# Optimization experiments

Hardware: AMD Instinct MI355X
Metric: run time of the kernel (lower is better)

## Reference

```python
import jax, jax.numpy as jnp
import numpy as np

B, N = 16, 512
CFL = 0.5


def _conv(x, k):
    return jax.lax.conv_general_dilated(x, k, (1, 1), 'VALID', dimension_numbers=('NHWC', 'HWIO', 'NHWC'))


def _pad(x, p):  # p = (top, bottom, left, right) spatial pads
    return jnp.pad(x, ((0, 0), (p[0], p[1]), (p[2], p[3]), (0, 0)))


def _t(k):  # transpose(perm=[1,0,2,3]) on an HWIO kernel
    return jnp.transpose(k, (1, 0, 2, 3))


def _amper(E, Hx, Hy, beta, delta, fb, fd, fy, kf, kb, fu, fdn):
    n = N
    s1 = (_pad(beta * _conv(Hy, _t(fb)) + delta * _conv(Hy, _t(fd)) + _conv(Hy, _t(fy)), (2, 2, 2, 2))
          + _pad(_conv(Hy, _t(kf)), (2, 2, 0, n - 1))
          + _pad(_conv(Hy, _t(kb)), (2, 2, n - 1, 0))
          + _pad(_conv(Hy, _t(fu)), (2, 2, 1, n - 2))
          + _pad(_conv(Hy, _t(fdn)), (2, 2, n - 2, 1)))
    s2 = (_pad(beta * _conv(Hx, fb) + delta * _conv(Hx, fd) + _conv(Hx, fy), (2, 2, 2, 2))
          + _pad(_conv(Hx, kf), (0, n - 1, 2, 2))
          + _pad(_conv(Hx, kb), (n - 1, 0, 2, 2))
          + _pad(_conv(Hx, fu), (1, n - 2, 2, 2))
          + _pad(_conv(Hx, fdn), (n - 2, 1, 2, 2)))
    return E + CFL * (s1 - s2)


def _faraday(E, Hx, Hy, beta, delta, fb, fd, fy, kef, keb):
    n = N
    s3 = (_pad(beta * _conv(E, fb) + delta * _conv(E, fd) + _conv(E, fy), (0, 0, 1, 1))
          + _pad(_conv(E, kef), (1, 1, 0, n - 2))[:, 1:-1, :, :]
          + _pad(_conv(E, keb), (1, 1, n - 2, 0))[:, 1:-1, :, :])
    s4 = (_pad(beta * _conv(E, _t(fb)) + delta * _conv(E, _t(fd)) + _conv(E, _t(fy)), (1, 1, 0, 0))
          + _pad(_conv(E, _t(kef)), (0, n - 2, 1, 1))[:, :, 1:-1, :]
          + _pad(_conv(E, _t(keb)), (n - 2, 0, 1, 1))[:, :, 1:-1, :])
    return Hx - CFL * s3, Hy + CFL * s4


def _forward(E1, Hx1, Hy1, beta, delta, fb, fd, fy, kf, kb, fu, fdn, kef, keb):
    E2 = _amper(E1, Hx1, Hy1, beta, delta, fb, fd, fy, kf, kb, fu, fdn)
    Hx2, Hy2 = _faraday(E2, Hx1, Hy1, beta, delta, fb, fd, fy, kef, keb)
    E3 = _amper(E2, Hx2, Hy2, beta, delta, fb, fd, fy, kf, kb, fu, fdn)
    Hx3, Hy3 = _faraday(E3, Hx2, Hy2, beta, delta, fb, fd, fy, kef, keb)
    E4 = _amper(E3, Hx3, Hy3, beta, delta, fb, fd, fy, kf, kb, fu, fdn)
    Hx4, Hy4 = _faraday(E4, Hx3, Hy3, beta, delta, fb, fd, fy, kef, keb)
    return (E2, Hx2, Hy2, E3, Hx3, Hy3, E4, Hx4, Hy4)


def setup_inputs():
    key = jax.random.key(0)
    ks = jax.random.split(key, 16)
    f32 = jnp.float32
    E_shape, Hx_shape, Hy_shape = (B, N + 1, N + 1, 1), (B, N - 1, N, 1), (B, N, N - 1, 1)
    # interior 2D DRP stencils (3x4): 4-tap staggered derivative x 3-tap transverse weights
    fy = np.zeros((3, 4, 1, 1), np.float32)
    fy[1, 1, 0, 0] = -1.0
    fy[1, 2, 0, 0] = 1.0
    fb = (np.outer([1.0, -2.0, 1.0], [0.0, -1.0, 1.0, 0.0]) / 8.0).astype(np.float32).reshape(3, 4, 1, 1)
    fd = (np.outer([0.0, 1.0, 0.0], [1.0, -3.0, 3.0, -1.0]) / 24.0).astype(np.float32).reshape(3, 4, 1, 1)
    rnd = lambda k, s: 0.05 * jax.random.normal(k, s, dtype=f32)
    return {
        'E1': jax.random.normal(ks[0], E_shape, f32),
        'Hx1': jax.random.normal(ks[1], Hx_shape, f32),
        'Hy1': jax.random.normal(ks[2], Hy_shape, f32),
        'E2': jax.random.normal(ks[3], E_shape, f32),
        'Hx2': jax.random.normal(ks[4], Hx_shape, f32),
        'Hy2': jax.random.normal(ks[5], Hy_shape, f32),
        'E3': jax.random.normal(ks[6], E_shape, f32),
        'Hx3': jax.random.normal(ks[7], Hx_shape, f32),
        'Hy3': jax.random.normal(ks[8], Hy_shape, f32),
        'beta': jnp.zeros((), f32),
        'delta': jnp.asarray([0.37], f32),
        'filter_beta': jnp.asarray(fb),
        'filter_delta': jnp.asarray(fd),
        'filter_yee': jnp.asarray(fy),
        'kernel_forward': rnd(ks[9], (N - 2, 4, 1, 1)),
        'kernel_backward': rnd(ks[10], (N - 2, 4, 1, 1)),
        'fourth_up': rnd(ks[11], (N - 2, 4, 1, 1)),
        'fourth_down': rnd(ks[12], (N - 2, 4, 1, 1)),
        'kernel_e_forward': rnd(ks[13], (3, N, 1, 1)),
        'kernel_e_backward': rnd(ks[14], (3, N, 1, 1)),
    }


def reference(E1, Hx1, Hy1, E2, Hx2, Hy2, E3, Hx3, Hy3, beta, delta, filter_beta, filter_delta, filter_yee, kernel_forward, kernel_backward, fourth_up, fourth_down, kernel_e_forward, kernel_e_backward):
    # Note: the original layer unpacks E2..Hy3 but never uses them.
    return _forward(E1, Hx1, Hy1, beta, delta, filter_beta, filter_delta, filter_yee,
                    kernel_forward, kernel_backward, fourth_up, fourth_down,
                    kernel_e_forward, kernel_e_backward)
```

## Files before the change

### kernel.cpp

```cpp
#include <hip/hip_runtime.h>

#define NB 16
#define NN 512
#define NP 513
#define NM 511
#define CFLc 0.5f

#define SE (NP*NP)
#define SHX (NM*NN)
#define SHY (NN*NM)

#define WS_BIG 0
#define WS_SMALL (16*16*6*512)
#define WS_TOT (WS_SMALL + 16*512*6)

__device__ __forceinline__ float dot4(float4 a, float4 b) {
    return a.x*b.x + a.y*b.y + a.z*b.z + a.w*b.w;
}

__device__ __forceinline__ void ld5(const float* __restrict__ a, int mb, float4* cr) {
    const float4* a4 = (const float4*)a;
    #pragma unroll
    for (int t = 0; t < 5; t++) {
        int idx = mb - 1 + t;
        if (idx >= 0 && idx <= 509) cr[t] = a4[idx];
        else cr[t] = make_float4(0.f, 0.f, 0.f, 0.f);
    }
}

__global__ __launch_bounds__(512, 4) void k_step1(
    const float* __restrict__ E, const float* __restrict__ Hx, const float* __restrict__ Hy,
    const float* __restrict__ beta, const float* __restrict__ delta,
    const float* __restrict__ fb, const float* __restrict__ fd, const float* __restrict__ fy,
    const float* __restrict__ kf, const float* __restrict__ kb,
    const float* __restrict__ fu, const float* __restrict__ fdn,
    float* __restrict__ ws, float* __restrict__ Eout)
{
    __shared__ float s_hy[7][512];
    __shared__ float s_hx[6][512];
    __shared__ float s_strip[8][6];
    __shared__ float gsm[12];

    int bid = blockIdx.x;
    int tid = threadIdx.x;

    if (bid < 256) {
        int b = bid >> 4;
        int chunk = bid & 15;
        int j = tid;
        if (j > 508) return;
        int p0 = chunk * 32;
        int p1 = min(510, p0 + 32);
        const float* Hxb = Hx + (size_t)b*SHX;
        float akf0=0,akf1=0,akb0=0,akb1=0,afu0=0,afu1=0,afd0=0,afd1=0;
        float r0v[4], r1v[4];
        #pragma unroll
        for (int q = 0; q < 4; q++) r0v[q] = Hxb[(size_t)p0*NN + j + q];
        for (int p = p0; p < p1; p++) {
            #pragma unroll
            for (int q = 0; q < 4; q++) r1v[q] = Hxb[(size_t)(p+1)*NN + j + q];
            #pragma unroll
            for (int q = 0; q < 4; q++) {
                float ckf = kf[p*4+q], ckb = kb[p*4+q], cfu = fu[p*4+q], cfd = fdn[p*4+q];
                akf0 += r0v[q]*ckf; akf1 += r1v[q]*ckf;
                akb0 += r0v[q]*ckb; akb1 += r1v[q]*ckb;
                afu0 += r0v[q]*cfu; afu1 += r1v[q]*cfu;
                afd0 += r0v[q]*cfd; afd1 += r1v[q]*cfd;
            }
            #pragma unroll
            for (int q = 0; q < 4; q++) r0v[q] = r1v[q];
        }
        float* o = ws + WS_BIG + (((size_t)b*16 + chunk)*6)*512 + j;
        o[0*512] = akf0;
        o[1*512] = akf1 + afu0;
        o[2*512] = afu1;
        o[3*512] = afd0;
        o[4*512] = afd1 + akb0;
        o[5*512] = akb1;
        return;
    }

    int wrk = bid - 256;
    wrk = (wrk & 7) * 258 + (wrk >> 3);
    int rg = wrk >> 4;
    int b  = wrk & 15;
    int r0 = rg * 4;

    const float* Eb  = E  + (size_t)b*SE;
    const float* Hxb = Hx + (size_t)b*SHX;
    const float* Hyb = Hy + (size_t)b*SHY;
    int c = tid;

    if (tid < 12) gsm[tid] = beta[0]*fb[tid] + delta[0]*fd[tid] + fy[tid];
    #pragma unroll
    for (int k = 0; k < 7; k++) {
        int rm = min(max(r0-2+k, 0), 511);
        s_hy[k][c] = Hyb[(size_t)rm*NM + min(c, 510)];
    }
    #pragma unroll
    for (int k = 0; k < 6; k++) {
        int rm = min(max(r0-2+k, 0), 510);
        s_hx[k][c] = Hxb[(size_t)rm*NN + c];
    }
    __syncthreads();

    {
        int w = tid >> 6, lane = tid & 63;
        int jj = w >> 1;
        int ii = r0 + jj - 2;
        if (ii >= 0 && ii <= 508) {
            int h = w & 1;
            int mb = h*256 + lane*4;
            float4 hv0 = *(const float4*)&s_hy[jj+0][mb];
            float4 hv1 = *(const float4*)&s_hy[jj+1][mb];
            float4 hv2 = *(const float4*)&s_hy[jj+2][mb];
            float4 hv3 = *(const float4*)&s_hy[jj+3][mb];
            float4 hc0 = make_float4(hv0.x, hv1.x, hv2.x, hv3.x);
            float4 hc1 = make_float4(hv0.y, hv1.y, hv2.y, hv3.y);
            float4 hc2 = make_float4(hv0.z, hv1.z, hv2.z, hv3.z);
            float4 hc3 = make_float4(hv0.w, hv1.w, hv2.w, hv3.w);
            float4 cr[5];
            ld5(kf, mb, cr);
            float pkf0 = dot4(hc0,cr[1]) + dot4(hc1,cr[2]) + dot4(hc2,cr[3]) + dot4(hc3,cr[4]);
            float pkf1 = dot4(hc0,cr[0]) + dot4(hc1,cr[1]) + dot4(hc2,cr[2]) + dot4(hc3,cr[3]);
            ld5(fu, mb, cr);
            float pfu0 = dot4(hc0,cr[1]) + dot4(hc1,cr[2]) + dot4(hc2,cr[3]) + dot4(hc3,cr[4]);
            float pfu1 = dot4(hc0,cr[0]) + dot4(hc1,cr[1]) + dot4(hc2,cr[2]) + dot4(hc3,cr[3]);
            ld5(fdn, mb, cr);
            float pfd0 = dot4(hc0,cr[1]) + dot4(hc1,cr[2]) + dot4(hc2,cr[3]) + dot4(hc3,cr[4]);
            float pfd1 = dot4(hc0,cr[0]) + dot4(hc1,cr[1]) + dot4(hc2,cr[2]) + dot4(hc3,cr[3]);
            ld5(kb, mb, cr);
            float pkb0 = dot4(hc0,cr[1]) + dot4(hc1,cr[2]) + dot4(hc2,cr[3]) + dot4(hc3,cr[4]);
            float pkb1 = dot4(hc0,cr[0]) + dot4(hc1,cr[1]) + dot4(hc2,cr[2]) + dot4(hc3,cr[3]);
            float v0 = pkf0;
            float v1 = pkf1 + pfu0;
            float v2 = pfu1;
            float v3 = pfd0;
            float v4 = pfd1 + pkb0;
            float v5 = pkb1;
            #pragma unroll
            for (int off = 32; off > 0; off >>= 1) {
                v0 += __shfl_down(v0, off);
                v1 += __shfl_down(v1, off);
                v2 += __shfl_down(v2, off);
                v3 += __shfl_down(v3, off);
                v4 += __shfl_down(v4, off);
                v5 += __shfl_down(v5, off);
            }
            if (lane == 0) {
                s_strip[w][0]=v0; s_strip[w][1]=v1; s_strip[w][2]=v2;
                s_strip[w][3]=v3; s_strip[w][4]=v4; s_strip[w][5]=v5;
            }
        }
    }
    __syncthreads();

    float g[12];
    #pragma unroll
    for (int i = 0; i < 12; i++) g[i] = gsm[i];

    int cy0 = min(max(c-2,0),510), cy1 = min(max(c-1,0),510), cy2 = min(c,510);
    int cx0 = max(c-2,0), cx1 = max(c-1,0), cx3 = min(c+1,511);
    float hyv[7][3];
    #pragma unroll
    for (int k = 0; k < 7; k++) {
        hyv[k][0]=s_hy[k][cy0]; hyv[k][1]=s_hy[k][cy1]; hyv[k][2]=s_hy[k][cy2];
    }
    float hxv[6][4];
    #pragma unroll
    for (int k = 0; k < 6; k++) {
        hxv[k][0]=s_hx[k][cx0]; hxv[k][1]=s_hx[k][cx1]; hxv[k][2]=s_hx[k][c]; hxv[k][3]=s_hx[k][cx3];
    }

    bool cint = (c >= 2 && c <= 510);
    int cslot = (c==0)?0:(c==1)?1:(c==2)?2:(c==510)?3:(c==511)?4:-1;
    float* Eo = Eout + (size_t)b*SE;

    #pragma unroll
    for (int j2 = 0; j2 < 4; j2++) {
        int r = r0 + j2;
        if (r > 512) break;
        float v = Eb[(size_t)r*NP + c];
        bool rint = (r >= 2 && r <= 510);
        if (rint && cint) {
            float s1 = 0.f, s2 = 0.f;
            #pragma unroll
            for (int p = 0; p < 4; p++)
                s1 += g[p]*hyv[j2+p][0] + g[4+p]*hyv[j2+p][1] + g[8+p]*hyv[j2+p][2];
            #pragma unroll
            for (int p = 0; p < 3; p++)
                s2 += g[p*4+0]*hxv[j2+p][0] + g[p*4+1]*hxv[j2+p][1]
                    + g[p*4+2]*hxv[j2+p][2] + g[p*4+3]*hxv[j2+p][3];
            v += CFLc * (s1 - s2);
        }
        if (rint && cslot >= 0)
            v += CFLc * (s_strip[2*j2][cslot] + s_strip[2*j2+1][cslot]);
        Eo[(size_t)r*NP + c] = v;
        if (c == 511) {
            float v2 = Eb[(size_t)r*NP + 512];
            if (rint) v2 += CFLc * (s_strip[2*j2][5] + s_strip[2*j2+1][5]);
            Eo[(size_t)r*NP + 512] = v2;
        }
    }
}

__global__ __launch_bounds__(512) void k_fix_e(
    const float* __restrict__ ws, float* __restrict__ Eout)
{
    int b = blockIdx.y;
    int which = blockIdx.x;
    int r = (which < 3) ? which : 507 + which;
    int c = 2 + threadIdx.x;
    if (c > 510) return;
    float s = 0.f;
    #pragma unroll
    for (int ch = 0; ch < 16; ch++)
        s += ws[WS_BIG + (((size_t)b*16 + ch)*6 + which)*512 + (c-2)];
    Eout[(size_t)b*SE + (size_t)r*NP + c] -= CFLc * s;
}

__global__ __launch_bounds__(512, 4) void k_step2(
    const float* __restrict__ E, const float* __restrict__ Hx, const float* __restrict__ Hy,
    const float* __restrict__ beta, const float* __restrict__ delta,
    const float* __restrict__ fb, const float* __restrict__ fd, const float* __restrict__ fy,
    const float* __restrict__ kef, const float* __restrict__ keb,
    float* __restrict__ ws, float* __restrict__ Hxout, float* __restrict__ Hyout)
{
    __shared__ float s_e[7][520];
    __shared__ float s_strip2[8][4];
    __shared__ float gsm[12];

    int bid = blockIdx.x;
    int tid = threadIdx.x;

    if (bid < 256) {
        int b = bid >> 4, chunk = bid & 15;
        int c = tid;
        if (c > 510) return;
        int p0 = chunk*32, p1 = p0 + 32;
        const float* Eb = E + (size_t)b*SE;
        float af0=0, af1=0, ab0=0, ab1=0;
        float r0v[3], r1v[3];
        #pragma unroll
        for (int q = 0; q < 3; q++) r0v[q] = Eb[(size_t)p0*NP + c + q];
        for (int p = p0; p < p1; p++) {
            #pragma unroll
            for (int q = 0; q < 3; q++) r1v[q] = Eb[(size_t)(p+1)*NP + c + q];
            float cf0 = kef[p], cf1 = kef[512+p], cf2 = kef[1024+p];
            float cb0 = keb[p], cb1 = keb[512+p], cb2 = keb[1024+p];
            af0 += r0v[0]*cf0 + r0v[1]*cf1 + r0v[2]*cf2;
            af1 += r1v[0]*cf0 + r1v[1]*cf1 + r1v[2]*cf2;
            ab0 += r0v[0]*cb0 + r0v[1]*cb1 + r0v[2]*cb2;
            ab1 += r1v[0]*cb0 + r1v[1]*cb1 + r1v[2]*cb2;
            r0v[0]=r1v[0]; r0v[1]=r1v[1]; r0v[2]=r1v[2];
        }
        float* o = ws + WS_BIG + (((size_t)b*16 + chunk)*4)*512 + c;
        o[0*512] = af0; o[1*512] = af1; o[2*512] = ab0; o[3*512] = ab1;
        return;
    }

    if (tid < 12) gsm[tid] = beta[0]*fb[tid] + delta[0]*fd[tid] + fy[tid];
    int c = tid;

    if (bid < 2304) {
        int wrk = bid - 256;
        wrk = (wrk & 7)*256 + (wrk >> 3);
        int y = wrk >> 4, b = wrk & 15;
        int r0 = y*4;
        const float* Eb = E + (size_t)b*SE;
        #pragma unroll
        for (int k = 0; k < 6; k++) {
            int rm = min(r0+k, 512);
            s_e[k][c] = Eb[(size_t)rm*NP + c];
            if (c == 511) s_e[k][512] = Eb[(size_t)rm*NP + 512];
        }
        __syncthreads();

        {
            int w = tid >> 6, lane = tid & 63;
            int jj = w >> 1, h = w & 1;
            int rr = r0 + jj;
            if (rr <= 510) {
                int mb = h*256 + lane*4;
                int q4 = mb >> 2;
                float4 e0 = *(const float4*)&s_e[jj+0][mb];
                float4 e1 = *(const float4*)&s_e[jj+1][mb];
                float4 e2 = *(const float4*)&s_e[jj+2][mb];
                const float4* kef4 = (const float4*)kef;
                const float4* keb4 = (const float4*)keb;
                float4 f0 = kef4[q4], f1 = kef4[128+q4], f2 = kef4[256+q4];
                float4 b0 = keb4[q4], b1 = keb4[128+q4], b2 = keb4[256+q4];
                float af0 = dot4(e0,f0) + dot4(e1,f1) + dot4(e2,f2);
                float ab0 = dot4(e0,b0) + dot4(e1,b1) + dot4(e2,b2);
                float pw0 = (mb >= 1) ? kef[mb-1]      : 0.f;
                float pw1 = (mb >= 1) ? kef[512+mb-1]  : 0.f;
                float pw2 = (mb >= 1) ? kef[1024+mb-1] : 0.f;
                float af1 = dot4(e0, make_float4(pw0, f0.x, f0.y, f0.z))
                          + dot4(e1, make_float4(pw1, f1.x, f1.y, f1.z))
                          + dot4(e2, make_float4(pw2, f2.x, f2.y, f2.z));
                pw0 = (mb >= 1) ? keb[mb-1]      : 0.f;
                pw1 = (mb >= 1) ? keb[512+mb-1]  : 0.f;
                pw2 = (mb >= 1) ? keb[1024+mb-1] : 0.f;
                float ab1 = dot4(e0, make_float4(pw0, b0.x, b0.y, b0.z))
                          + dot4(e1, make_float4(pw1, b1.x, b1.y, b1.z))
                          + dot4(e2, make_float4(pw2, b2.x, b2.y, b2.z));
                if (mb == 508) {
                    float e512_0 = s_e[jj+0][512];
                    float e512_1 = s_e[jj+1][512];
                    float e512_2 = s_e[jj+2][512];
                    af1 += e512_0*kef[511] + e512_1*kef[1023] + e512_2*kef[1535];
                    ab1 += e512_0*keb[511] + e512_1*keb[1023] + e512_2*keb[1535];
                }
                #pragma unroll
                for (int off = 32; off > 0; off >>= 1) {
                    af0 += __shfl_down(af0, off);
                    af1 += __shfl_down(af1, off);
                    ab0 += __shfl_down(ab0, off);
                    ab1 += __shfl_down(ab1, off);
                }
                if (lane == 0) {
                    s_strip2[w][0]=af0; s_strip2[w][1]=af1;
                    s_strip2[w][2]=ab0; s_strip2[w][3]=ab1;
                }
            }
        }
        __syncthreads();

        float g[12];
        #pragma unroll
        for (int i = 0; i < 12; i++) g[i] = gsm[i];
        int c0 = max(c-1,0), c2i = min(c+1,512), c3i = min(c+2,512);
        float ev[6][4];
        #pragma unroll
        for (int k = 0; k < 6; k++) {
            ev[k][0]=s_e[k][c0]; ev[k][1]=s_e[k][c]; ev[k][2]=s_e[k][c2i]; ev[k][3]=s_e[k][c3i];
        }
        bool cint = (c >= 1 && c <= 510);
        int slot = (c==0)?0:(c==1)?1:(c==510)?2:(c==511)?3:-1;
        const float* Hxb = Hx + (size_t)b*SHX;
        float* Ho = Hxout + (size_t)b*SHX;
        #pragma unroll
        for (int j2 = 0; j2 < 4; j2++) {
            int r = r0 + j2;
            if (r > 510) break;
            float v = Hxb[(size_t)r*NN + c];
            if (cint) {
                float s = 0.f;
                #pragma unroll
                for (int p = 0; p < 3; p++)
                    s += g[p*4+0]*ev[j2+p][0] + g[p*4+1]*ev[j2+p][1]
                       + g[p*4+2]*ev[j2+p][2] + g[p*4+3]*ev[j2+p][3];
                v -= CFLc * s;
            }
            if (slot >= 0)
                v -= CFLc * (s_strip2[2*j2][slot] + s_strip2[2*j2+1][slot]);
            Ho[(size_t)r*NN + c] = v;
        }
    } else {
        int wrk = bid - 2304;
        wrk = (wrk & 7)*256 + (wrk >> 3);
        int y = wrk >> 4, b = wrk & 15;
        int r0 = y*4;
        const float* Eb = E + (size_t)b*SE;
        #pragma unroll
        for (int k = 0; k < 7; k++) {
            int rm = min(max(r0-1+k, 0), 512);
            s_e[k][c] = Eb[(size_t)rm*NP + c];
            if (c == 511) s_e[k][512] = Eb[(size_t)rm*NP + 512];
        }
        __syncthreads();
        if (c > 510) return;

        float g[12];
        #pragma unroll
        for (int i = 0; i < 12; i++) g[i] = gsm[i];
        float ev[7][3];
        #pragma unroll
        for (int k = 0; k < 7; k++) {
            ev[k][0]=s_e[k][c]; ev[k][1]=s_e[k][c+1]; ev[k][2]=s_e[k][c+2];
        }
        const float* Hyb = Hy + (size_t)b*SHY;
        float* Ho = Hyout + (size_t)b*SHY;
        #pragma unroll
        for (int j2 = 0; j2 < 4; j2++) {
            int r = r0 + j2;
            float v = Hyb[(size_t)r*NM + c];
            if (r >= 1 && r <= 510) {
                float s = 0.f;
                #pragma unroll
                for (int p = 0; p < 4; p++)
                    s += g[p]*ev[j2+p][0] + g[4+p]*ev[j2+p][1] + g[8+p]*ev[j2+p][2];
                v += CFLc * s;
            }
            Ho[(size_t)r*NM + c] = v;
        }
    }
}

__global__ __launch_bounds__(512) void k_fix_hy(
    const float* __restrict__ ws, float* __restrict__ Hyout)
{
    int b = blockIdx.y;
    int which = blockIdx.x;
    int r = (which < 2) ? which : 508 + which;
    int c = threadIdx.x;
    if (c > 510) return;
    float s = 0.f;
    #pragma unroll
    for (int ch = 0; ch < 16; ch++)
        s += ws[WS_BIG + (((size_t)b*16 + ch)*4 + which)*512 + c];
    Hyout[(size_t)b*SHY + (size_t)r*NM + c] += CFLc * s;
}


static void run_step(const float* Ein, const float* Hxin, const float* Hyin,
                     float* Eout, float* Hxout, float* Hyout, float* ws,
                     const float* beta, const float* delta,
                     const float* fb, const float* fd, const float* fy,
                     const float* kf, const float* kb, const float* fu, const float* fdn,
                     const float* kef, const float* keb, hipStream_t stream)
{
    dim3 blk(512);
    k_step1<<<dim3(256 + 2064), blk, 0, stream>>>(Ein, Hxin, Hyin, beta, delta,
        fb, fd, fy, kf, kb, fu, fdn, ws, Eout);
    k_fix_e<<<dim3(6, NB), blk, 0, stream>>>(ws, Eout);
    k_step2<<<dim3(256 + 2048 + 2048), blk, 0, stream>>>(Eout, Hxin, Hyin, beta, delta,
        fb, fd, fy, kef, keb, ws, Hxout, Hyout);
    k_fix_hy<<<dim3(4, NB), blk, 0, stream>>>(ws, Hyout);
}

extern "C" void kernel_launch(void* const* d_in, const int* in_sizes, int n_in,
                              void* d_out, int out_size, void* d_ws, size_t ws_size,
                              hipStream_t stream)
{
    const float* E1   = (const float*)d_in[0];
    const float* Hx1  = (const float*)d_in[1];
    const float* Hy1  = (const float*)d_in[2];
    const float* beta = (const float*)d_in[9];
    const float* delta= (const float*)d_in[10];
    const float* fb   = (const float*)d_in[11];
    const float* fd   = (const float*)d_in[12];
    const float* fy   = (const float*)d_in[13];
    const float* kf   = (const float*)d_in[14];
    const float* kb   = (const float*)d_in[15];
    const float* fu   = (const float*)d_in[16];
    const float* fdn  = (const float*)d_in[17];
    const float* kef  = (const float*)d_in[18];
    const float* keb  = (const float*)d_in[19];

    float* out = (float*)d_out;
    float* ws  = (float*)d_ws;
    size_t SEa = (size_t)NB * SE;
    size_t SHa = (size_t)NB * SHX;
    float* E2  = out;
    float* Hx2 = E2  + SEa;
    float* Hy2 = Hx2 + SHa;
    float* E3  = Hy2 + SHa;
    float* Hx3 = E3  + SEa;
    float* Hy3 = Hx3 + SHa;
    float* E4  = Hy3 + SHa;
    float* Hx4 = E4  + SEa;
    float* Hy4 = Hx4 + SHa;

    run_step(E1, Hx1, Hy1, E2, Hx2, Hy2, ws, beta, delta, fb, fd, fy, kf, kb, fu, fdn, kef, keb, stream);
    run_step(E2, Hx2, Hy2, E3, Hx3, Hy3, ws, beta, delta, fb, fd, fy, kf, kb, fu, fdn, kef, keb, stream);
    run_step(E3, Hx3, Hy3, E4, Hx4, Hy4, ws, beta, delta, fb, fd, fy, kf, kb, fu, fdn, kef, keb, stream);
}
```

Measured before the change: 485.7 us.

## Fold boundary fix-up kernels into following step kernels and merge Hx/Hy blocks

Removes the separate k_fix_e and k_fix_hy launches. Boundary strip values are stashed in workspace and the pending long-range corrections are applied on the fly by the next kernel that reads them, plus dedicated tail blocks that write the final fixed rows. It also halves the number of long-range reduction chunks (8 instead of 16, each covering twice as many rows), and merges the separate Hx and Hy block sets in k_step2 so one block computes both from a shared E tile. This cuts launches and duplicated E loads, at the cost of more complex indexing, more serial work per reduction block, and a risk of ordering errors on the boundary rows.

```diff
diff --git a/kernel.cpp b/kernel.cpp
--- a/kernel.cpp
+++ b/kernel.cpp
@@ -10,9 +10,15 @@
 #define SHX (NM*NN)
 #define SHY (NN*NM)
 
-#define WS_BIG 0
-#define WS_SMALL (16*16*6*512)
-#define WS_TOT (WS_SMALL + 16*512*6)
+#define NCH 8
+#define OFF_A 0
+#define SZ_A (NB*NCH*6*512)
+#define OFF_F (OFF_A + SZ_A)
+#define SZ_F (NB*NCH*4*512)
+#define OFF_SE (OFF_F + SZ_F)
+#define SZ_SE (NB*6*NP)
+#define OFF_SH (OFF_SE + SZ_SE)
+#define SZ_SH (NB*4*NM)
 
 __device__ __forceinline__ float dot4(float4 a, float4 b) {
     return a.x*b.x + a.y*b.y + a.z*b.z + a.w*b.w;
@@ -34,7 +40,8 @@
     const float* __restrict__ fb, const float* __restrict__ fd, const float* __restrict__ fy,
     const float* __restrict__ kf, const float* __restrict__ kb,
     const float* __restrict__ fu, const float* __restrict__ fdn,
-    float* __restrict__ ws, float* __restrict__ Eout)
+    float* __restrict__ ws, float* __restrict__ Eout,
+    float* __restrict__ Hyfix, int fix)
 {
     __shared__ float s_hy[7][512];
     __shared__ float s_hx[6][512];
@@ -44,13 +51,13 @@
     int bid = blockIdx.x;
     int tid = threadIdx.x;
 
-    if (bid < 256) {
-        int b = bid >> 4;
-        int chunk = bid & 15;
+    if (bid < 128) {
+        int b = bid >> 3;
+        int chunk = bid & 7;
         int j = tid;
         if (j > 508) return;
-        int p0 = chunk * 32;
-        int p1 = min(510, p0 + 32);
+        int p0 = chunk * 64;
+        int p1 = min(510, p0 + 64);
         const float* Hxb = Hx + (size_t)b*SHX;
         float akf0=0,akf1=0,akb0=0,akb1=0,afu0=0,afu1=0,afd0=0,afd1=0;
         float r0v[4], r1v[4];
@@ -70,7 +77,7 @@
             #pragma unroll
             for (int q = 0; q < 4; q++) r0v[q] = r1v[q];
         }
-        float* o = ws + WS_BIG + (((size_t)b*16 + chunk)*6)*512 + j;
+        float* o = ws + OFF_A + (((size_t)b*NCH + chunk)*6)*512 + j;
         o[0*512] = akf0;
         o[1*512] = akf1 + afu0;
         o[2*512] = afu1;
@@ -80,7 +87,25 @@
         return;
     }
 
-    int wrk = bid - 256;
+    if (bid >= 2192) {
+        if (!fix) return;
+        int b = bid - 2192;
+        int c = tid;
+        if (c > 510) return;
+        #pragma unroll
+        for (int slot = 0; slot < 4; slot++) {
+            int r = (slot < 2) ? slot : 508 + slot;
+            float s = 0.f;
+            #pragma unroll
+            for (int ch = 0; ch < NCH; ch++)
+                s += ws[OFF_F + (((size_t)b*NCH + ch)*4 + slot)*512 + c];
+            Hyfix[(size_t)b*SHY + (size_t)r*NM + c] =
+                ws[OFF_SH + ((size_t)b*4 + slot)*NM + c] + CFLc*s;
+        }
+        return;
+    }
+
+    int wrk = bid - 128;
     wrk = (wrk & 7) * 258 + (wrk >> 3);
     int rg = wrk >> 4;
     int b  = wrk & 15;
@@ -95,7 +120,19 @@
     #pragma unroll
     for (int k = 0; k < 7; k++) {
         int rm = min(max(r0-2+k, 0), 511);
-        s_hy[k][c] = Hyb[(size_t)rm*NM + min(c, 510)];
+        int cc = min(c, 510);
+        float v;
+        if (fix && (rm <= 1 || rm >= 510)) {
+            int slot = (rm <= 1) ? rm : rm - 508;
+            float s = 0.f;
+            #pragma unroll
+            for (int ch = 0; ch < NCH; ch++)
+                s += ws[OFF_F + (((size_t)b*NCH + ch)*4 + slot)*512 + cc];
+            v = ws[OFF_SH + ((size_t)b*4 + slot)*NM + cc] + CFLc*s;
+        } else {
+            v = Hyb[(size_t)rm*NM + cc];
+        }
+        s_hy[k][c] = v;
     }
     #pragma unroll
     for (int k = 0; k < 6; k++) {
@@ -196,27 +233,18 @@
         if (rint && cslot >= 0)
             v += CFLc * (s_strip[2*j2][cslot] + s_strip[2*j2+1][cslot]);
         Eo[(size_t)r*NP + c] = v;
+        bool rstrip = (r <= 2 || r >= 510);
+        int rslot = (r <= 2) ? r : r - 507;
+        if (rstrip)
+            ws[OFF_SE + ((size_t)b*6 + rslot)*NP + c] = v;
         if (c == 511) {
             float v2 = Eb[(size_t)r*NP + 512];
             if (rint) v2 += CFLc * (s_strip[2*j2][5] + s_strip[2*j2+1][5]);
             Eo[(size_t)r*NP + 512] = v2;
-        }
-    }
-}
-
-__global__ __launch_bounds__(512) void k_fix_e(
-    const float* __restrict__ ws, float* __restrict__ Eout)
-{
-    int b = blockIdx.y;
-    int which = blockIdx.x;
-    int r = (which < 3) ? which : 507 + which;
-    int c = 2 + threadIdx.x;
-    if (c > 510) return;
-    float s = 0.f;
-    #pragma unroll
-    for (int ch = 0; ch < 16; ch++)
-        s += ws[WS_BIG + (((size_t)b*16 + ch)*6 + which)*512 + (c-2)];
-    Eout[(size_t)b*SE + (size_t)r*NP + c] -= CFLc * s;
+            if (rstrip)
+                ws[OFF_SE + ((size_t)b*6 + rslot)*NP + 512] = v2;
+        }
+    }
 }
 
 __global__ __launch_bounds__(512, 4) void k_step2(
@@ -224,28 +252,56 @@
     const float* __restrict__ beta, const float* __restrict__ delta,
     const float* __restrict__ fb, const float* __restrict__ fd, const float* __restrict__ fy,
     const float* __restrict__ kef, const float* __restrict__ keb,
-    float* __restrict__ ws, float* __restrict__ Hxout, float* __restrict__ Hyout)
+    float* __restrict__ ws, float* __restrict__ Hxout, float* __restrict__ Hyout,
+    float* __restrict__ Efix)
 {
     __shared__ float s_e[7][520];
+    __shared__ float s_fix[3][NP];
     __shared__ float s_strip2[8][4];
     __shared__ float gsm[12];
 
     int bid = blockIdx.x;
     int tid = threadIdx.x;
 
-    if (bid < 256) {
-        int b = bid >> 4, chunk = bid & 15;
+    if (bid < 128) {
+        int b = bid >> 3, chunk = bid & 7;
+        const float* Eb = E + (size_t)b*SE;
+        bool bnd = (chunk == 0 || chunk == 7);
+        int rbase = (chunk == 0) ? 0 : 510;
+        if (bnd) {
+            int sbase = (chunk == 0) ? 0 : 3;
+            for (int t = tid; t < 3*NP; t += 512) {
+                int sr = t / NP, cc = t - sr*NP;
+                int slot = sbase + sr;
+                float v = ws[OFF_SE + ((size_t)b*6 + slot)*NP + cc];
+                if (cc >= 2 && cc <= 510) {
+                    float s = 0.f;
+                    #pragma unroll
+                    for (int ch = 0; ch < NCH; ch++)
+                        s += ws[OFF_A + (((size_t)b*NCH + ch)*6 + slot)*512 + (cc-2)];
+                    v -= CFLc * s;
+                }
+                s_fix[sr][cc] = v;
+            }
+            __syncthreads();
+        }
         int c = tid;
         if (c > 510) return;
-        int p0 = chunk*32, p1 = p0 + 32;
-        const float* Eb = E + (size_t)b*SE;
+        int p0 = chunk*64, p1 = p0 + 64;
+        auto ldE = [&](int rr, int col) -> float {
+            if (bnd) {
+                unsigned d = (unsigned)(rr - rbase);
+                if (d < 3u) return s_fix[d][col];
+            }
+            return Eb[(size_t)rr*NP + col];
+        };
         float af0=0, af1=0, ab0=0, ab1=0;
         float r0v[3], r1v[3];
         #pragma unroll
-        for (int q = 0; q < 3; q++) r0v[q] = Eb[(size_t)p0*NP + c + q];
+        for (int q = 0; q < 3; q++) r0v[q] = ldE(p0, c + q);
         for (int p = p0; p < p1; p++) {
             #pragma unroll
-            for (int q = 0; q < 3; q++) r1v[q] = Eb[(size_t)(p+1)*NP + c + q];
+            for (int q = 0; q < 3; q++) r1v[q] = ldE(p+1, c + q);
             float cf0 = kef[p], cf1 = kef[512+p], cf2 = kef[1024+p];
             float cb0 = keb[p], cb1 = keb[512+p], cb2 = keb[1024+p];
             af0 += r0v[0]*cf0 + r0v[1]*cf1 + r0v[2]*cf2;
@@ -254,78 +310,114 @@
             ab1 += r1v[0]*cb0 + r1v[1]*cb1 + r1v[2]*cb2;
             r0v[0]=r1v[0]; r0v[1]=r1v[1]; r0v[2]=r1v[2];
         }
-        float* o = ws + WS_BIG + (((size_t)b*16 + chunk)*4)*512 + c;
+        float* o = ws + OFF_F + (((size_t)b*NCH + chunk)*4)*512 + c;
         o[0*512] = af0; o[1*512] = af1; o[2*512] = ab0; o[3*512] = ab1;
         return;
     }
 
+    if (bid >= 2176) {
+        int b = bid - 2176;
+        int c = tid;
+        if (c < 2 || c > 510) return;
+        #pragma unroll
+        for (int slot = 0; slot < 6; slot++) {
+            int r = (slot < 3) ? slot : 507 + slot;
+            float s = 0.f;
+            #pragma unroll
+            for (int ch = 0; ch < NCH; ch++)
+                s += ws[OFF_A + (((size_t)b*NCH + ch)*6 + slot)*512 + (c-2)];
+            Efix[(size_t)b*SE + (size_t)r*NP + c] =
+                ws[OFF_SE + ((size_t)b*6 + slot)*NP + c] - CFLc*s;
+        }
+        return;
+    }
+
     if (tid < 12) gsm[tid] = beta[0]*fb[tid] + delta[0]*fd[tid] + fy[tid];
+    int wrk = bid - 128;
+    wrk = (wrk & 7)*256 + (wrk >> 3);
+    int y = wrk >> 4, b = wrk & 15;
+    int r0 = y*4;
+    const float* Eb = E + (size_t)b*SE;
     int c = tid;
 
-    if (bid < 2304) {
-        int wrk = bid - 256;
-        wrk = (wrk & 7)*256 + (wrk >> 3);
-        int y = wrk >> 4, b = wrk & 15;
-        int r0 = y*4;
-        const float* Eb = E + (size_t)b*SE;
-        #pragma unroll
-        for (int k = 0; k < 6; k++) {
-            int rm = min(r0+k, 512);
-            s_e[k][c] = Eb[(size_t)rm*NP + c];
-            if (c == 511) s_e[k][512] = Eb[(size_t)rm*NP + 512];
-        }
-        __syncthreads();
-
-        {
-            int w = tid >> 6, lane = tid & 63;
-            int jj = w >> 1, h = w & 1;
-            int rr = r0 + jj;
-            if (rr <= 510) {
-                int mb = h*256 + lane*4;
-                int q4 = mb >> 2;
-                float4 e0 = *(const float4*)&s_e[jj+0][mb];
-                float4 e1 = *(const float4*)&s_e[jj+1][mb];
-                float4 e2 = *(const float4*)&s_e[jj+2][mb];
-                const float4* kef4 = (const float4*)kef;
-                const float4* keb4 = (const float4*)keb;
-                float4 f0 = kef4[q4], f1 = kef4[128+q4], f2 = kef4[256+q4];
-                float4 b0 = keb4[q4], b1 = keb4[128+q4], b2 = keb4[256+q4];
-                float af0 = dot4(e0,f0) + dot4(e1,f1) + dot4(e2,f2);
-                float ab0 = dot4(e0,b0) + dot4(e1,b1) + dot4(e2,b2);
-                float pw0 = (mb >= 1) ? kef[mb-1]      : 0.f;
-                float pw1 = (mb >= 1) ? kef[512+mb-1]  : 0.f;
-                float pw2 = (mb >= 1) ? kef[1024+mb-1] : 0.f;
-                float af1 = dot4(e0, make_float4(pw0, f0.x, f0.y, f0.z))
-                          + dot4(e1, make_float4(pw1, f1.x, f1.y, f1.z))
-                          + dot4(e2, make_float4(pw2, f2.x, f2.y, f2.z));
-                pw0 = (mb >= 1) ? keb[mb-1]      : 0.f;
-                pw1 = (mb >= 1) ? keb[512+mb-1]  : 0.f;
-                pw2 = (mb >= 1) ? keb[1024+mb-1] : 0.f;
-                float ab1 = dot4(e0, make_float4(pw0, b0.x, b0.y, b0.z))
-                          + dot4(e1, make_float4(pw1, b1.x, b1.y, b1.z))
-                          + dot4(e2, make_float4(pw2, b2.x, b2.y, b2.z));
-                if (mb == 508) {
-                    float e512_0 = s_e[jj+0][512];
-                    float e512_1 = s_e[jj+1][512];
-                    float e512_2 = s_e[jj+2][512];
-                    af1 += e512_0*kef[511] + e512_1*kef[1023] + e512_2*kef[1535];
-                    ab1 += e512_0*keb[511] + e512_1*keb[1023] + e512_2*keb[1535];
-                }
+    #pragma unroll
+    for (int k = 0; k < 7; k++) {
+        int rm = min(max(r0-1+k, 0), 512);
+        bool strip = (rm <= 2 || rm >= 510);
+        int slot = (rm <= 2) ? rm : rm - 507;
+        float v;
+        if (strip) {
+            v = ws[OFF_SE + ((size_t)b*6 + slot)*NP + c];
+            if (c >= 2 && c <= 510) {
+                float s = 0.f;
                 #pragma unroll
-                for (int off = 32; off > 0; off >>= 1) {
-                    af0 += __shfl_down(af0, off);
-                    af1 += __shfl_down(af1, off);
-                    ab0 += __shfl_down(ab0, off);
-                    ab1 += __shfl_down(ab1, off);
-                }
-                if (lane == 0) {
-                    s_strip2[w][0]=af0; s_strip2[w][1]=af1;
-                    s_strip2[w][2]=ab0; s_strip2[w][3]=ab1;
-                }
-            }
-        }
-        __syncthreads();
-
+                for (int ch = 0; ch < NCH; ch++)
+                    s += ws[OFF_A + (((size_t)b*NCH + ch)*6 + slot)*512 + (c-2)];
+                v -= CFLc * s;
+            }
+        } else {
+            v = Eb[(size_t)rm*NP + c];
+        }
+        s_e[k][c] = v;
+        if (c == 511) {
+            float v2 = strip ? ws[OFF_SE + ((size_t)b*6 + slot)*NP + 512]
+                             : Eb[(size_t)rm*NP + 512];
+            s_e[k][512] = v2;
+        }
+    }
+    __syncthreads();
+
+    {
+        int w = tid >> 6, lane = tid & 63;
+        int jj = w >> 1, h = w & 1;
+        int rr = r0 + jj;
+        if (rr <= 510) {
+            int mb = h*256 + lane*4;
+            int q4 = mb >> 2;
+            float4 e0 = *(const float4*)&s_e[jj+1][mb];
+            float4 e1 = *(const float4*)&s_e[jj+2][mb];
+            float4 e2 = *(const float4*)&s_e[jj+3][mb];
+            const float4* kef4 = (const float4*)kef;
+            const float4* keb4 = (const float4*)keb;
+            float4 f0 = kef4[q4], f1 = kef4[128+q4], f2 = kef4[256+q4];
+            float4 b0 = keb4[q4], b1 = keb4[128+q4], b2 = keb4[256+q4];
+            float af0 = dot4(e0,f0) + dot4(e1,f1) + dot4(e2,f2);
+            float ab0 = dot4(e0,b0) + dot4(e1,b1) + dot4(e2,b2);
+            float pw0 = (mb >= 1) ? kef[mb-1]      : 0.f;
+            float pw1 = (mb >= 1) ? kef[512+mb-1]  : 0.f;
+            float pw2 = (mb >= 1) ? kef[1024+mb-1] : 0.f;
+            float af1 = dot4(e0, make_float4(pw0, f0.x, f0.y, f0.z))
+                      + dot4(e1, make_float4(pw1, f1.x, f1.y, f1.z))
+                      + dot4(e2, make_float4(pw2, f2.x, f2.y, f2.z));
+            pw0 = (mb >= 1) ? keb[mb-1]      : 0.f;
+            pw1 = (mb >= 1) ? keb[512+mb-1]  : 0.f;
+            pw2 = (mb >= 1) ? keb[1024+mb-1] : 0.f;
+            float ab1 = dot4(e0, make_float4(pw0, b0.x, b0.y, b0.z))
+                      + dot4(e1, make_float4(pw1, b1.x, b1.y, b1.z))
+                      + dot4(e2, make_float4(pw2, b2.x, b2.y, b2.z));
+            if (mb == 508) {
+                float e512_0 = s_e[jj+1][512];
+                float e512_1 = s_e[jj+2][512];
+                float e512_2 = s_e[jj+3][512];
+                af1 += e512_0*kef[511] + e512_1*kef[1023] + e512_2*kef[1535];
+                ab1 += e512_0*keb[511] + e512_1*keb[1023] + e512_2*keb[1535];
+            }
+            #pragma unroll
+            for (int off = 32; off > 0; off >>= 1) {
+                af0 += __shfl_down(af0, off);
+                af1 += __shfl_down(af1, off);
+                ab0 += __shfl_down(ab0, off);
+                ab1 += __shfl_down(ab1, off);
+            }
+            if (lane == 0) {
+                s_strip2[w][0]=af0; s_strip2[w][1]=af1;
+                s_strip2[w][2]=ab0; s_strip2[w][3]=ab1;
+            }
+        }
+    }
+    __syncthreads();
+
+    {
         float g[12];
         #pragma unroll
         for (int i = 0; i < 12; i++) g[i] = gsm[i];
@@ -333,7 +425,8 @@
         float ev[6][4];
         #pragma unroll
         for (int k = 0; k < 6; k++) {
-            ev[k][0]=s_e[k][c0]; ev[k][1]=s_e[k][c]; ev[k][2]=s_e[k][c2i]; ev[k][3]=s_e[k][c3i];
+            ev[k][0]=s_e[k+1][c0]; ev[k][1]=s_e[k+1][c];
+            ev[k][2]=s_e[k+1][c2i]; ev[k][3]=s_e[k+1][c3i];
         }
         bool cint = (c >= 1 && c <= 510);
         int slot = (c==0)?0:(c==1)?1:(c==510)?2:(c==511)?3:-1;
@@ -356,21 +449,9 @@
                 v -= CFLc * (s_strip2[2*j2][slot] + s_strip2[2*j2+1][slot]);
             Ho[(size_t)r*NN + c] = v;
         }
-    } else {
-        int wrk = bid - 2304;
-        wrk = (wrk & 7)*256 + (wrk >> 3);
-        int y = wrk >> 4, b = wrk & 15;
-        int r0 = y*4;
-        const float* Eb = E + (size_t)b*SE;
-        #pragma unroll
-        for (int k = 0; k < 7; k++) {
-            int rm = min(max(r0-1+k, 0), 512);
-            s_e[k][c] = Eb[(size_t)rm*NP + c];
-            if (c == 511) s_e[k][512] = Eb[(size_t)rm*NP + 512];
-        }
-        __syncthreads();
-        if (c > 510) return;
-
+    }
+
+    if (c <= 510) {
         float g[12];
         #pragma unroll
         for (int i = 0; i < 12; i++) g[i] = gsm[i];
@@ -393,23 +474,28 @@
                 v += CFLc * s;
             }
             Ho[(size_t)r*NM + c] = v;
-        }
-    }
-}
-
-__global__ __launch_bounds__(512) void k_fix_hy(
+            if (r <= 1 || r >= 510)
+                ws[OFF_SH + ((size_t)b*4 + ((r<=1)?r:r-508))*NM + c] = v;
+        }
+    }
+}
+
+__global__ __launch_bounds__(512) void k_fix_hy_final(
     const float* __restrict__ ws, float* __restrict__ Hyout)
 {
-    int b = blockIdx.y;
-    int which = blockIdx.x;
-    int r = (which < 2) ? which : 508 + which;
+    int b = blockIdx.x;
     int c = threadIdx.x;
     if (c > 510) return;
-    float s = 0.f;
-    #pragma unroll
-    for (int ch = 0; ch < 16; ch++)
-        s += ws[WS_BIG + (((size_t)b*16 + ch)*4 + which)*512 + c];
-    Hyout[(size_t)b*SHY + (size_t)r*NM + c] += CFLc * s;
+    #pragma unroll
+    for (int slot = 0; slot < 4; slot++) {
+        int r = (slot < 2) ? slot : 508 + slot;
+        float s = 0.f;
+        #pragma unroll
+        for (int ch = 0; ch < NCH; ch++)
+            s += ws[OFF_F + (((size_t)b*NCH + ch)*4 + slot)*512 + c];
+        Hyout[(size_t)b*SHY + (size_t)r*NM + c] =
+            ws[OFF_SH + ((size_t)b*4 + slot)*NM + c] + CFLc*s;
+    }
 }
 
 
@@ -418,15 +504,14 @@
                      const float* beta, const float* delta,
                      const float* fb, const float* fd, const float* fy,
                      const float* kf, const float* kb, const float* fu, const float* fdn,
-                     const float* kef, const float* keb, hipStream_t stream)
+                     const float* kef, const float* keb,
+                     float* HyfixTarget, int fix, hipStream_t stream)
 {
     dim3 blk(512);
-    k_step1<<<dim3(256 + 2064), blk, 0, stream>>>(Ein, Hxin, Hyin, beta, delta,
-        fb, fd, fy, kf, kb, fu, fdn, ws, Eout);
-    k_fix_e<<<dim3(6, NB), blk, 0, stream>>>(ws, Eout);
-    k_step2<<<dim3(256 + 2048 + 2048), blk, 0, stream>>>(Eout, Hxin, Hyin, beta, delta,
-        fb, fd, fy, kef, keb, ws, Hxout, Hyout);
-    k_fix_hy<<<dim3(4, NB), blk, 0, stream>>>(ws, Hyout);
+    k_step1<<<dim3(2208), blk, 0, stream>>>(Ein, Hxin, Hyin, beta, delta,
+        fb, fd, fy, kf, kb, fu, fdn, ws, Eout, HyfixTarget, fix);
+    k_step2<<<dim3(2192), blk, 0, stream>>>(Eout, Hxin, Hyin, beta, delta,
+        fb, fd, fy, kef, keb, ws, Hxout, Hyout, Eout);
 }
 
 extern "C" void kernel_launch(void* const* d_in, const int* in_sizes, int n_in,
@@ -462,7 +547,11 @@
     float* Hx4 = E4  + SEa;
     float* Hy4 = Hx4 + SHa;
 
-    run_step(E1, Hx1, Hy1, E2, Hx2, Hy2, ws, beta, delta, fb, fd, fy, kf, kb, fu, fdn, kef, keb, stream);
-    run_step(E2, Hx2, Hy2, E3, Hx3, Hy3, ws, beta, delta, fb, fd, fy, kf, kb, fu, fdn, kef, keb, stream);
-    run_step(E3, Hx3, Hy3, E4, Hx4, Hy4, ws, beta, delta, fb, fd, fy, kf, kb, fu, fdn, kef, keb, stream);
-}
+    run_step(E1, Hx1, Hy1, E2, Hx2, Hy2, ws, beta, delta, fb, fd, fy,
+             kf, kb, fu, fdn, kef, keb, nullptr, 0, stream);
+    run_step(E2, Hx2, Hy2, E3, Hx3, Hy3, ws, beta, delta, fb, fd, fy,
+             kf, kb, fu, fdn, kef, keb, Hy2, 1, stream);
+    run_step(E3, Hx3, Hy3, E4, Hx4, Hy4, ws, beta, delta, fb, fd, fy,
+             kf, kb, fu, fdn, kef, keb, Hy3, 1, stream);
+    k_fix_hy_final<<<dim3(16), dim3(512), 0, stream>>>(ws, Hy4);
+}
```

Measured after the change: 502.3 us. +3.4%, slower.
